# Kernel tuning notes

Hardware: AMD Instinct MI355X
Metric: run time of the kernel (lower is better)

The kernel has to match this reference:

```python
import jax, jax.numpy as jnp
import numpy as np
from jax import lax

S, L = 8192, 16
N_WORD, N_CHAR = 50000, 128
WORD_DIM, CHAR_DIM = 256, 64
WORD_HID, CHAR_HID = 512, 128
N_TAG = 64


def _lstm_gates(x, h, Wih, Whh, bih, bhh):
    # x: [..., D], h: [..., H]; torch gate order: i, f, g, o
    g = x @ Wih.T + h @ Whh.T + bih + bhh
    i, f, gg, o = jnp.split(g, 4, axis=-1)
    return jax.nn.sigmoid(i), jax.nn.sigmoid(f), jnp.tanh(gg), jax.nn.sigmoid(o)


def setup_inputs() -> dict:
    key = jax.random.key(0)
    ks = jax.random.split(key, 16)
    sc = 0.1
    inp = {
        'x': jax.random.randint(ks[0], (S,), 0, N_WORD),
        'chars': jax.random.randint(ks[1], (S, L), 0, N_CHAR),
        'lengths': jax.random.randint(ks[2], (S,), 0, L),
        'word_emb': jax.random.normal(ks[3], (N_WORD, WORD_DIM), jnp.float32) * sc,
        'char_emb': jax.random.normal(ks[4], (N_CHAR, CHAR_DIM), jnp.float32) * sc,
        'c_Wih': jax.random.normal(ks[5], (4 * CHAR_HID, CHAR_DIM), jnp.float32) * sc,
        'c_Whh': jax.random.normal(ks[6], (4 * CHAR_HID, CHAR_HID), jnp.float32) * sc,
        'c_bih': jax.random.normal(ks[7], (4 * CHAR_HID,), jnp.float32) * sc,
        'c_bhh': jax.random.normal(ks[8], (4 * CHAR_HID,), jnp.float32) * sc,
        'w_Wih': jax.random.normal(ks[9], (4 * WORD_HID, WORD_DIM + CHAR_HID), jnp.float32) * sc,
        'w_Whh': jax.random.normal(ks[10], (4 * WORD_HID, WORD_HID), jnp.float32) * sc,
        'w_bih': jax.random.normal(ks[11], (4 * WORD_HID,), jnp.float32) * sc,
        'w_bhh': jax.random.normal(ks[12], (4 * WORD_HID,), jnp.float32) * sc,
        'lin_W': jax.random.normal(ks[13], (N_TAG, WORD_HID), jnp.float32) * sc,
        'lin_b': jax.random.normal(ks[14], (N_TAG,), jnp.float32) * sc,
    }
    return inp


def _char_features(chars, lengths, char_emb, Wih, Whh, bih, bhh):
    # batched char LSTM over all S words at once; returns final CELL state (h[1] in torch)
    emb = char_emb[chars]              # [S, L, char_dim]
    xs = jnp.swapaxes(emb, 0, 1)       # [L, S, char_dim]
    h0 = jnp.zeros((chars.shape[0], CHAR_HID), emb.dtype)
    c0 = jnp.zeros_like(h0)

    def step(carry, inp):
        h, c = carry
        x_t, t = inp
        i, f, g, o = _lstm_gates(x_t, h, Wih, Whh, bih, bhh)
        c_new = f * c + i * g
        h_new = o * jnp.tanh(c_new)
        m = (t < lengths)[:, None]     # only update within each word's true length
        return (jnp.where(m, h_new, h), jnp.where(m, c_new, c)), None

    (h, c), _ = lax.scan(step, (h0, c0), (xs, jnp.arange(L)))
    return c                            # [S, char_hidden]


def _word_lstm(seq, Wih, Whh, bih, bhh):
    # seq: [S, D] single sequence (batch=1 in original)
    h0 = jnp.zeros((WORD_HID,), seq.dtype)
    c0 = jnp.zeros_like(h0)

    def step(carry, x_t):
        h, c = carry
        i, f, g, o = _lstm_gates(x_t, h, Wih, Whh, bih, bhh)
        c = f * c + i * g
        h = o * jnp.tanh(c)
        return (h, c), h

    _, hs = lax.scan(step, (h0, c0), seq)
    return hs                           # [S, word_hidden]


def reference(x, chars, lengths, word_emb, char_emb,
              c_Wih, c_Whh, c_bih, c_bhh,
              w_Wih, w_Whh, w_bih, w_bhh,
              lin_W, lin_b):
    char_feat = _char_features(chars, lengths, char_emb, c_Wih, c_Whh, c_bih, c_bhh)
    we = word_emb[x]                                    # [S, word_dim]
    seq = jnp.concatenate([we, char_feat], axis=1)      # [S, word_dim+char_hidden]
    hs = _word_lstm(seq, w_Wih, w_Whh, w_bih, w_bhh)    # [S, word_hidden]
    logits = hs @ lin_W.T + lin_b                       # [S, n_tag]
    return jax.nn.log_softmax(logits, axis=1)
```

## Files before the change

### kernel.cpp

```cpp
#include <hip/hip_runtime.h>
#include <hip/hip_bf16.h>

#define S_LEN 8192
#define CLEN 16
#define WDIM 256
#define CDIM 64
#define CHID 128
#define WHID 512
#define GDIM 2048
#define NTAG 64
#define KDIM 384
#define NWG 32

typedef unsigned long long u64;

__device__ __forceinline__ float sigmoidf_(float x) {
  return 1.0f / (1.0f + __expf(-x));
}
__device__ __forceinline__ float tanhf_(float x) {
  return 1.0f - 2.0f / (__expf(2.0f * x) + 1.0f);
}

__global__ __launch_bounds__(256)
void char_lstm_kernel(const int* __restrict__ chars, const int* __restrict__ lengths,
                      const float* __restrict__ emb, const float* __restrict__ Wih,
                      const float* __restrict__ Whh, const float* __restrict__ bih,
                      const float* __restrict__ bhh, float* __restrict__ cf)
{
  __shared__ float xs[16][CDIM];
  __shared__ float hsm[16][CHID];
  __shared__ int cidx[16];
  __shared__ int lens[16];
  const int tid = threadIdx.x;
  const int grp = tid >> 7;
  const int j = tid & 127;
  const int wb = blockIdx.x * 16;

  for (int i = tid; i < 16 * CHID; i += 256) (&hsm[0][0])[i] = 0.f;
  if (tid < 16) lens[tid] = lengths[wb + tid];
  float c[8];
#pragma unroll
  for (int w = 0; w < 8; ++w) c[w] = 0.f;
  const float bi = bih[j] + bhh[j];
  const float bf = bih[CHID + j] + bhh[CHID + j];
  const float bg = bih[2 * CHID + j] + bhh[2 * CHID + j];
  const float bo = bih[3 * CHID + j] + bhh[3 * CHID + j];

  for (int t = 0; t < CLEN; ++t) {
    __syncthreads();
    if (tid < 16) cidx[tid] = chars[(wb + tid) * CLEN + t];
    __syncthreads();
    {
      int e = tid * 4;
      int wi = e >> 6;
      int k = e & 63;
      const float4 v = *(const float4*)(emb + (size_t)cidx[wi] * CDIM + k);
      *(float4*)(&xs[wi][k]) = v;
    }
    __syncthreads();
    float ai[8], af[8], ag[8], ao[8];
#pragma unroll
    for (int w = 0; w < 8; ++w) { ai[w] = bi; af[w] = bf; ag[w] = bg; ao[w] = bo; }
    for (int k = 0; k < CDIM; k += 4) {
      float4 w0 = *(const float4*)(Wih + (size_t)j * CDIM + k);
      float4 w1 = *(const float4*)(Wih + (size_t)(CHID + j) * CDIM + k);
      float4 w2 = *(const float4*)(Wih + (size_t)(2 * CHID + j) * CDIM + k);
      float4 w3 = *(const float4*)(Wih + (size_t)(3 * CHID + j) * CDIM + k);
#pragma unroll
      for (int s = 0; s < 4; ++s) {
        float wiv = (&w0.x)[s], wfv = (&w1.x)[s], wgv = (&w2.x)[s], wov = (&w3.x)[s];
#pragma unroll
        for (int w = 0; w < 8; ++w) {
          float xv = xs[grp * 8 + w][k + s];
          ai[w] = fmaf(wiv, xv, ai[w]);
          af[w] = fmaf(wfv, xv, af[w]);
          ag[w] = fmaf(wgv, xv, ag[w]);
          ao[w] = fmaf(wov, xv, ao[w]);
        }
      }
    }
    for (int k = 0; k < CHID; k += 4) {
      float4 w0 = *(const float4*)(Whh + (size_t)j * CHID + k);
      float4 w1 = *(const float4*)(Whh + (size_t)(CHID + j) * CHID + k);
      float4 w2 = *(const float4*)(Whh + (size_t)(2 * CHID + j) * CHID + k);
      float4 w3 = *(const float4*)(Whh + (size_t)(3 * CHID + j) * CHID + k);
#pragma unroll
      for (int s = 0; s < 4; ++s) {
        float wiv = (&w0.x)[s], wfv = (&w1.x)[s], wgv = (&w2.x)[s], wov = (&w3.x)[s];
#pragma unroll
        for (int w = 0; w < 8; ++w) {
          float hv = hsm[grp * 8 + w][k + s];
          ai[w] = fmaf(wiv, hv, ai[w]);
          af[w] = fmaf(wfv, hv, af[w]);
          ag[w] = fmaf(wgv, hv, ag[w]);
          ao[w] = fmaf(wov, hv, ao[w]);
        }
      }
    }
    __syncthreads();
#pragma unroll
    for (int w = 0; w < 8; ++w) {
      if (t < lens[grp * 8 + w]) {
        float iv = sigmoidf_(ai[w]);
        float fv = sigmoidf_(af[w]);
        float gv = tanhf_(ag[w]);
        float ov = sigmoidf_(ao[w]);
        c[w] = fv * c[w] + iv * gv;
        hsm[grp * 8 + w][j] = ov * tanhf_(c[w]);
      }
    }
  }
#pragma unroll
  for (int w = 0; w < 8; ++w)
    cf[(size_t)(wb + grp * 8 + w) * CHID + j] = c[w];
}

#define BM 64
#define BN 64
#define BK 32
__global__ __launch_bounds__(256)
void gx_gemm_kernel(const int* __restrict__ x, const float* __restrict__ word_emb,
                    const float* __restrict__ char_feat, const float* __restrict__ Wih,
                    const float* __restrict__ bih, const float* __restrict__ bhh,
                    float* __restrict__ Gx)
{
  __shared__ float As[BK][BM + 1];
  __shared__ float Bs[BK][BN + 1];
  __shared__ int xidx[BM];
  const int tid = threadIdx.x;
  const int tx = tid & 15, ty = tid >> 4;
  const int m0 = blockIdx.y * BM;
  const int n0 = blockIdx.x * BN;
  if (tid < BM) xidx[tid] = x[m0 + tid];
  float acc[4][4] = {};
  for (int k0 = 0; k0 < KDIM; k0 += BK) {
    __syncthreads();
    {
      int i = tid >> 5;
      int kk = tid & 31;
#pragma unroll
      for (int l = 0; l < 8; ++l) {
        int row = i + l * 8;
        int k = k0 + kk;
        int tt = m0 + row;
        float v = (k < WDIM) ? word_emb[(size_t)xidx[row] * WDIM + k]
                             : char_feat[(size_t)tt * CHID + (k - WDIM)];
        As[kk][row] = v;
      }
    }
    {
      int jjj = tid >> 5;
      int kk = tid & 31;
#pragma unroll
      for (int l = 0; l < 8; ++l) {
        int col = jjj + l * 8;
        Bs[kk][col] = Wih[(size_t)(n0 + col) * KDIM + k0 + kk];
      }
    }
    __syncthreads();
#pragma unroll
    for (int kk = 0; kk < BK; ++kk) {
      float a[4], b[4];
#pragma unroll
      for (int m = 0; m < 4; ++m) a[m] = As[kk][ty * 4 + m];
#pragma unroll
      for (int n = 0; n < 4; ++n) b[n] = Bs[kk][tx * 4 + n];
#pragma unroll
      for (int m = 0; m < 4; ++m)
#pragma unroll
        for (int n = 0; n < 4; ++n)
          acc[m][n] = fmaf(a[m], b[n], acc[m][n]);
    }
  }
#pragma unroll
  for (int n = 0; n < 4; ++n) {
    int g = n0 + tx * 4 + n;
    float bias = bih[g] + bhh[g];
#pragma unroll
    for (int m = 0; m < 4; ++m) {
      int tt = m0 + ty * 4 + m;
      Gx[(size_t)tt * GDIM + g] = acc[m][n] + bias;
    }
  }
}

__global__ __launch_bounds__(256, 1)
void word_lstm_seq(const float* __restrict__ Whh, const float* __restrict__ Gx,
                   float* __restrict__ hs, u64* hbuf)
{
  __shared__ float h_lds[WHID];
  __shared__ float red[2][256];
  const int tid = threadIdx.x;
  const int wg = blockIdx.x;
  const int cc = tid >> 6;
  const int lane = tid & 63;
  const int kb = cc * 128;

  const int grow = (lane >> 4) * WHID + wg * 16 + (lane & 15);
  float wl[128];
  {
    const float* wsrc = Whh + (size_t)grow * WHID + kb;
#pragma unroll
    for (int k = 0; k < 128; ++k) wl[k] = wsrc[k];
  }

  float c_state = 0.f;

  for (int t = 0; t < S_LEN; ++t) {
    float gxv = 0.f;
    if (tid < 64)
      gxv = Gx[(size_t)t * GDIM + grow];
    if (t > 0) {
      const u64* base = hbuf + (size_t)(t & 1) * WHID + kb;
      const int s0 = 2 * lane;
      u64 a, b;
      const unsigned want = (unsigned)t;
      while (true) {
        a = __hip_atomic_load(base + s0, __ATOMIC_RELAXED,
                              __HIP_MEMORY_SCOPE_AGENT);
        b = __hip_atomic_load(base + s0 + 1, __ATOMIC_RELAXED,
                              __HIP_MEMORY_SCOPE_AGENT);
        if ((unsigned)(a >> 32) == want && (unsigned)(b >> 32) == want) break;
      }
      float2 hv2 = make_float2(__uint_as_float((unsigned)a),
                               __uint_as_float((unsigned)b));
      *(float2*)(&h_lds[kb + s0]) = hv2;
    } else {
      *(float2*)(&h_lds[kb + 2 * lane]) = make_float2(0.f, 0.f);
    }
    __threadfence_block();
    float acc = 0.f;
#pragma unroll
    for (int g = 0; g < 32; ++g) {
      float4 hv = *(const float4*)(&h_lds[kb + 4 * g]);
      acc = fmaf(wl[4 * g + 0], hv.x, acc);
      acc = fmaf(wl[4 * g + 1], hv.y, acc);
      acc = fmaf(wl[4 * g + 2], hv.z, acc);
      acc = fmaf(wl[4 * g + 3], hv.w, acc);
    }
    red[t & 1][tid] = acc;
    __syncthreads();
    if (tid < 64) {
      const float* rp = &red[t & 1][0];
      float s = rp[tid] + rp[64 + tid] + rp[128 + tid] + rp[192 + tid] + gxv;
      float act = ((tid >> 4) == 2) ? tanhf_(s) : sigmoidf_(s);
      int jj = tid & 15;
      float iv = __shfl(act, jj);
      float fv = __shfl(act, 16 + jj);
      float gv = __shfl(act, 32 + jj);
      float ov = __shfl(act, 48 + jj);
      if (tid < 16) {
        c_state = fv * c_state + iv * gv;
        float hv = ov * tanhf_(c_state);
        const int hidx = wg * 16 + tid;
        u64 pkt = ((u64)(unsigned)(t + 1) << 32) | (u64)__float_as_uint(hv);
        (void)__hip_atomic_exchange(
            &hbuf[(size_t)((t + 1) & 1) * WHID + hidx], pkt,
            __ATOMIC_RELAXED, __HIP_MEMORY_SCOPE_AGENT);
        hs[(size_t)t * WHID + hidx] = hv;
      }
    }
  }
}

__global__ __launch_bounds__(256)
void tag_kernel(const float* __restrict__ hs, const float* __restrict__ W,
                const float* __restrict__ b, float* __restrict__ out)
{
  const int wave = threadIdx.x >> 6;
  const int lane = threadIdx.x & 63;
  const int t = blockIdx.x * 4 + wave;
  const float* hr = hs + (size_t)t * WHID;
  const float* wr = W + (size_t)lane * WHID;
  float acc = b[lane];
  for (int k = 0; k < WHID; k += 4) {
    float4 wv = *(const float4*)(wr + k);
    float4 hv = *(const float4*)(hr + k);
    acc = fmaf(wv.x, hv.x, acc);
    acc = fmaf(wv.y, hv.y, acc);
    acc = fmaf(wv.z, hv.z, acc);
    acc = fmaf(wv.w, hv.w, acc);
  }
  float m = acc;
#pragma unroll
  for (int off = 32; off > 0; off >>= 1) m = fmaxf(m, __shfl_xor(m, off));
  float e = __expf(acc - m);
  float sum = e;
#pragma unroll
  for (int off = 32; off > 0; off >>= 1) sum += __shfl_xor(sum, off);
  out[(size_t)t * NTAG + lane] = (acc - m) - __logf(sum);
}

extern "C" void kernel_launch(void* const* d_in, const int* in_sizes, int n_in,
                              void* d_out, int out_size, void* d_ws, size_t ws_size,
                              hipStream_t stream)
{
  const int* x          = (const int*)d_in[0];
  const int* chars      = (const int*)d_in[1];
  const int* lengths    = (const int*)d_in[2];
  const float* word_emb = (const float*)d_in[3];
  const float* char_emb = (const float*)d_in[4];
  const float* c_Wih    = (const float*)d_in[5];
  const float* c_Whh    = (const float*)d_in[6];
  const float* c_bih    = (const float*)d_in[7];
  const float* c_bhh    = (const float*)d_in[8];
  const float* w_Wih    = (const float*)d_in[9];
  const float* w_Whh    = (const float*)d_in[10];
  const float* w_bih    = (const float*)d_in[11];
  const float* w_bhh    = (const float*)d_in[12];
  const float* lin_W    = (const float*)d_in[13];
  const float* lin_b    = (const float*)d_in[14];
  float* out = (float*)d_out;

  char* ws = (char*)d_ws;
  u64*   hbuf      = (u64*)ws;
  float* char_feat = (float*)(ws + 8192);
  float* Gx        = (float*)(ws + 8192 + (size_t)S_LEN * CHID * 4);
  float* hs        = (float*)(ws + 8192 + (size_t)S_LEN * CHID * 4
                                        + (size_t)S_LEN * GDIM * 4);

  hipMemsetAsync(ws, 0, 8192, stream);

  char_lstm_kernel<<<S_LEN / 16, 256, 0, stream>>>(
      chars, lengths, char_emb, c_Wih, c_Whh, c_bih, c_bhh, char_feat);

  dim3 g2(GDIM / BN, S_LEN / BM);
  gx_gemm_kernel<<<g2, 256, 0, stream>>>(
      x, word_emb, char_feat, w_Wih, w_bih, w_bhh, Gx);

  word_lstm_seq<<<NWG, 256, 0, stream>>>(w_Whh, Gx, hs, hbuf);

  tag_kernel<<<S_LEN / 4, 256, 0, stream>>>(hs, lin_W, lin_b, out);
}
```

Baseline: 15.86 ms.

## Restructure word LSTM recurrence so each wave owns full gate rows with shuffle reduction

Measured after the change: 19.80 ms. 24.9% more time.

```diff
diff --git a/kernel.cpp b/kernel.cpp
--- a/kernel.cpp
+++ b/kernel.cpp
@@ -188,77 +188,80 @@
 void word_lstm_seq(const float* __restrict__ Whh, const float* __restrict__ Gx,
                    float* __restrict__ hs, u64* hbuf)
 {
-  __shared__ float h_lds[WHID];
-  __shared__ float red[2][256];
-  const int tid = threadIdx.x;
-  const int wg = blockIdx.x;
-  const int cc = tid >> 6;
+  __shared__ __align__(16) float stg[2][640];
+  const int tid  = threadIdx.x;
+  const int wg   = blockIdx.x;
+  const int wv   = tid >> 6;
   const int lane = tid & 63;
-  const int kb = cc * 128;
-
-  const int grow = (lane >> 4) * WHID + wg * 16 + (lane & 15);
-  float wl[128];
+  const int kc   = lane >> 4;
+  const int r    = lane & 15;
+  const int q    = r >> 2;
+  const int u    = r & 3;
+  const int grow = q * WHID + wg * 16 + wv * 4 + u;
+
+  float4 w_[32];
   {
-    const float* wsrc = Whh + (size_t)grow * WHID + kb;
-#pragma unroll
-    for (int k = 0; k < 128; ++k) wl[k] = wsrc[k];
+    const float* wsrc = Whh + (size_t)grow * WHID + 128 * kc;
+#pragma unroll
+    for (int i = 0; i < 32; ++i) {
+      const int fo = (4 * kc + 4 * i) & 127;
+      w_[i] = *(const float4*)(wsrc + fo);
+    }
+#pragma unroll
+    for (int i = 0; i < 32; ++i)
+      asm volatile("" : "+v"(w_[i].x), "+v"(w_[i].y), "+v"(w_[i].z), "+v"(w_[i].w));
   }
 
   float c_state = 0.f;
 
   for (int t = 0; t < S_LEN; ++t) {
-    float gxv = 0.f;
-    if (tid < 64)
-      gxv = Gx[(size_t)t * GDIM + grow];
+    const int par = t & 1;
+    float gxv = Gx[(size_t)t * GDIM + grow];
+    float v0, v1;
     if (t > 0) {
-      const u64* base = hbuf + (size_t)(t & 1) * WHID + kb;
-      const int s0 = 2 * lane;
+      const u64* pb = hbuf + (size_t)par * WHID + 128 * wv + 2 * lane;
+      const unsigned want = (unsigned)t;
       u64 a, b;
-      const unsigned want = (unsigned)t;
-      while (true) {
-        a = __hip_atomic_load(base + s0, __ATOMIC_RELAXED,
-                              __HIP_MEMORY_SCOPE_AGENT);
-        b = __hip_atomic_load(base + s0 + 1, __ATOMIC_RELAXED,
-                              __HIP_MEMORY_SCOPE_AGENT);
-        if ((unsigned)(a >> 32) == want && (unsigned)(b >> 32) == want) break;
-      }
-      float2 hv2 = make_float2(__uint_as_float((unsigned)a),
-                               __uint_as_float((unsigned)b));
-      *(float2*)(&h_lds[kb + s0]) = hv2;
-    } else {
-      *(float2*)(&h_lds[kb + 2 * lane]) = make_float2(0.f, 0.f);
-    }
-    __threadfence_block();
+      do {
+        a = __hip_atomic_load(pb + 0, __ATOMIC_RELAXED, __HIP_MEMORY_SCOPE_AGENT);
+        b = __hip_atomic_load(pb + 1, __ATOMIC_RELAXED, __HIP_MEMORY_SCOPE_AGENT);
+      } while (((unsigned)(a >> 32) != want) | ((unsigned)(b >> 32) != want));
+      v0 = __uint_as_float((unsigned)a);
+      v1 = __uint_as_float((unsigned)b);
+    } else { v0 = 0.f; v1 = 0.f; }
+    {
+      float* cb = &stg[par][148 * wv];
+      *(float2*)(cb + 2 * lane) = make_float2(v0, v1);
+      if (lane < 6) *(float2*)(cb + 128 + 2 * lane) = make_float2(v0, v1);
+    }
+    __syncthreads();
+    const float* rdp = &stg[par][152 * kc];
     float acc = 0.f;
 #pragma unroll
-    for (int g = 0; g < 32; ++g) {
-      float4 hv = *(const float4*)(&h_lds[kb + 4 * g]);
-      acc = fmaf(wl[4 * g + 0], hv.x, acc);
-      acc = fmaf(wl[4 * g + 1], hv.y, acc);
-      acc = fmaf(wl[4 * g + 2], hv.z, acc);
-      acc = fmaf(wl[4 * g + 3], hv.w, acc);
-    }
-    red[t & 1][tid] = acc;
-    __syncthreads();
-    if (tid < 64) {
-      const float* rp = &red[t & 1][0];
-      float s = rp[tid] + rp[64 + tid] + rp[128 + tid] + rp[192 + tid] + gxv;
-      float act = ((tid >> 4) == 2) ? tanhf_(s) : sigmoidf_(s);
-      int jj = tid & 15;
-      float iv = __shfl(act, jj);
-      float fv = __shfl(act, 16 + jj);
-      float gv = __shfl(act, 32 + jj);
-      float ov = __shfl(act, 48 + jj);
-      if (tid < 16) {
-        c_state = fv * c_state + iv * gv;
-        float hv = ov * tanhf_(c_state);
-        const int hidx = wg * 16 + tid;
-        u64 pkt = ((u64)(unsigned)(t + 1) << 32) | (u64)__float_as_uint(hv);
-        (void)__hip_atomic_exchange(
-            &hbuf[(size_t)((t + 1) & 1) * WHID + hidx], pkt,
-            __ATOMIC_RELAXED, __HIP_MEMORY_SCOPE_AGENT);
-        hs[(size_t)t * WHID + hidx] = hv;
-      }
+    for (int i = 0; i < 32; ++i) {
+      const float4 hv = *(const float4*)(rdp + 4 * i);
+      acc = fmaf(w_[i].x, hv.x, acc);
+      acc = fmaf(w_[i].y, hv.y, acc);
+      acc = fmaf(w_[i].z, hv.z, acc);
+      acc = fmaf(w_[i].w, hv.w, acc);
+    }
+    acc += __shfl_xor(acc, 16);
+    acc += __shfl_xor(acc, 32);
+    const float s = acc + gxv;
+    const float act = (q == 2) ? tanhf_(s) : sigmoidf_(s);
+    const int gb = lane & 48;
+    const float iv = __shfl(act, gb + u);
+    const float fv = __shfl(act, gb + 4 + u);
+    const float gv = __shfl(act, gb + 8 + u);
+    const float ov = __shfl(act, gb + 12 + u);
+    c_state = fv * c_state + iv * gv;
+    const float hv = ov * tanhf_(c_state);
+    if (lane < 4) {
+      const int hidx = wg * 16 + wv * 4 + lane;
+      const u64 pkt = ((u64)(unsigned)(t + 1) << 32) | (u64)__float_as_uint(hv);
+      (void)__hip_atomic_exchange(&hbuf[(size_t)((t + 1) & 1) * WHID + hidx], pkt,
+                                  __ATOMIC_RELAXED, __HIP_MEMORY_SCOPE_AGENT);
+      hs[(size_t)t * WHID + hidx] = hv;
     }
   }
 }
```

## Race redundant XCC-local LSTM replicas against global group for faster h exchange

Applied to the files above, without the earlier changes.

Measured after the change: 17.90 ms. 1.13x slower.

```diff
diff --git a/kernel.cpp b/kernel.cpp
--- a/kernel.cpp
+++ b/kernel.cpp
@@ -186,80 +186,186 @@
 
 __global__ __launch_bounds__(256, 1)
 void word_lstm_seq(const float* __restrict__ Whh, const float* __restrict__ Gx,
-                   float* __restrict__ hs, u64* hbuf)
+                   float* __restrict__ hs, u64* hbufG, u64* hbufL,
+                   int* tickets, int* done_cnt, int* done)
 {
+  __shared__ __align__(16) float4 wlds[4096];
   __shared__ float h_lds[WHID];
   __shared__ float red[2][256];
+  __shared__ int wg_s, loc_s, bail_s;
   const int tid = threadIdx.x;
-  const int wg = blockIdx.x;
-  const int cc = tid >> 6;
+  const int bid = blockIdx.x;
+
+  if (tid == 0) {
+    bail_s = 0;
+    int myid, loc;
+    if (bid < NWG) {
+      myid = bid; loc = -1;
+    } else {
+      unsigned xcc;
+      asm volatile("s_getreg_b32 %0, hwreg(HW_REG_XCC_ID)" : "=s"(xcc));
+      xcc &= 15u;
+      int tk = __hip_atomic_fetch_add(&tickets[xcc], 1, __ATOMIC_RELAXED,
+                                      __HIP_MEMORY_SCOPE_AGENT);
+      myid = -1; loc = (int)xcc;
+      if (tk < NWG) {
+        for (int i = 0; i < 30000; ++i) {
+          if (__hip_atomic_load(&tickets[xcc], __ATOMIC_RELAXED,
+                                __HIP_MEMORY_SCOPE_AGENT) >= NWG) {
+            myid = tk; break;
+          }
+        }
+      }
+    }
+    wg_s = myid; loc_s = loc;
+  }
+  __syncthreads();
+  const int wg = wg_s;
+  if (wg < 0) return;
+  const bool local = (loc_s >= 0);
+  u64* __restrict__ mybuf = local ? (hbufL + (size_t)loc_s * 1024) : hbufG;
+
+  const int cc   = tid >> 6;
   const int lane = tid & 63;
-  const int kb = cc * 128;
-
+  const int kb   = cc * 128;
   const int grow = (lane >> 4) * WHID + wg * 16 + (lane & 15);
-  float wl[128];
+
+  for (int L = tid; L < 4096; L += 256) {
+    int g = L >> 8;
+    int rem = L & 255;
+    int c2 = rem >> 6;
+    int r = rem & 63;
+    int gr = (r >> 4) * WHID + wg * 16 + (r & 15);
+    wlds[L] = *(const float4*)(Whh + (size_t)gr * WHID + c2 * 128 + 4 * g);
+  }
+  float4 wr_[16];
   {
-    const float* wsrc = Whh + (size_t)grow * WHID + kb;
-#pragma unroll
-    for (int k = 0; k < 128; ++k) wl[k] = wsrc[k];
-  }
+    const float* wsrc2 = Whh + (size_t)grow * WHID + kb + 64;
+#pragma unroll
+    for (int i = 0; i < 16; ++i) wr_[i] = *(const float4*)(wsrc2 + 4 * i);
+  }
+  __syncthreads();
 
   float c_state = 0.f;
+  int lmode = local ? 1 : 0;
 
   for (int t = 0; t < S_LEN; ++t) {
+    const int par = t & 1;
     float gxv = 0.f;
     if (tid < 64)
       gxv = Gx[(size_t)t * GDIM + grow];
+    float v0 = 0.f, v1 = 0.f;
     if (t > 0) {
-      const u64* base = hbuf + (size_t)(t & 1) * WHID + kb;
-      const int s0 = 2 * lane;
-      u64 a, b;
       const unsigned want = (unsigned)t;
-      while (true) {
-        a = __hip_atomic_load(base + s0, __ATOMIC_RELAXED,
-                              __HIP_MEMORY_SCOPE_AGENT);
-        b = __hip_atomic_load(base + s0 + 1, __ATOMIC_RELAXED,
-                              __HIP_MEMORY_SCOPE_AGENT);
-        if ((unsigned)(a >> 32) == want && (unsigned)(b >> 32) == want) break;
-      }
-      float2 hv2 = make_float2(__uint_as_float((unsigned)a),
-                               __uint_as_float((unsigned)b));
-      *(float2*)(&h_lds[kb + s0]) = hv2;
-    } else {
-      *(float2*)(&h_lds[kb + 2 * lane]) = make_float2(0.f, 0.f);
-    }
+      const size_t soff = (size_t)par * WHID + kb + 2 * lane;
+      bool found = false;
+      if (lmode) {
+        const u64* pL = mybuf + soff;
+        int iter = 0;
+        for (;;) {
+          int4 rr;
+          asm volatile("global_load_dwordx4 %0, %1, off sc0\n\t"
+                       "s_waitcnt vmcnt(0)"
+                       : "=v"(rr) : "v"(pL) : "memory");
+          if ((unsigned)rr.y == want && (unsigned)rr.w == want) {
+            v0 = __int_as_float(rr.x); v1 = __int_as_float(rr.z);
+            found = true; break;
+          }
+          ++iter;
+          if (t == 1 && iter >= 4096) { lmode = 0; break; }
+          if ((iter & 15) == 0 &&
+              __hip_atomic_load(done, __ATOMIC_RELAXED,
+                                __HIP_MEMORY_SCOPE_AGENT)) {
+            bail_s = 1; found = true; break;
+          }
+        }
+      }
+      if (!found) {
+        const u64* pG = hbufG + soff;
+        const u64* pL = mybuf + soff;
+        int iter = 0;
+        for (;;) {
+          u64 a = __hip_atomic_load(pG + 0, __ATOMIC_RELAXED,
+                                    __HIP_MEMORY_SCOPE_AGENT);
+          u64 b = __hip_atomic_load(pG + 1, __ATOMIC_RELAXED,
+                                    __HIP_MEMORY_SCOPE_AGENT);
+          if ((unsigned)(a >> 32) == want && (unsigned)(b >> 32) == want) {
+            v0 = __uint_as_float((unsigned)a);
+            v1 = __uint_as_float((unsigned)b);
+            break;
+          }
+          if (local) {
+            int4 rr;
+            asm volatile("global_load_dwordx4 %0, %1, off sc0\n\t"
+                         "s_waitcnt vmcnt(0)"
+                         : "=v"(rr) : "v"(pL) : "memory");
+            if ((unsigned)rr.y == want && (unsigned)rr.w == want) {
+              v0 = __int_as_float(rr.x); v1 = __int_as_float(rr.z); break;
+            }
+          }
+          if (((++iter) & 15) == 0 &&
+              __hip_atomic_load(done, __ATOMIC_RELAXED,
+                                __HIP_MEMORY_SCOPE_AGENT)) {
+            bail_s = 1; break;
+          }
+        }
+      }
+    }
+    *(float2*)(&h_lds[kb + 2 * lane]) = make_float2(v0, v1);
     __threadfence_block();
     float acc = 0.f;
 #pragma unroll
-    for (int g = 0; g < 32; ++g) {
-      float4 hv = *(const float4*)(&h_lds[kb + 4 * g]);
-      acc = fmaf(wl[4 * g + 0], hv.x, acc);
-      acc = fmaf(wl[4 * g + 1], hv.y, acc);
-      acc = fmaf(wl[4 * g + 2], hv.z, acc);
-      acc = fmaf(wl[4 * g + 3], hv.w, acc);
-    }
-    red[t & 1][tid] = acc;
-    __syncthreads();
+    for (int g = 0; g < 16; ++g) {
+      const float4 wv = wlds[g * 256 + cc * 64 + lane];
+      const float4 hv = *(const float4*)(&h_lds[kb + 4 * g]);
+      acc = fmaf(wv.x, hv.x, acc);
+      acc = fmaf(wv.y, hv.y, acc);
+      acc = fmaf(wv.z, hv.z, acc);
+      acc = fmaf(wv.w, hv.w, acc);
+    }
+#pragma unroll
+    for (int i = 0; i < 16; ++i) {
+      const float4 hv = *(const float4*)(&h_lds[kb + 64 + 4 * i]);
+      acc = fmaf(wr_[i].x, hv.x, acc);
+      acc = fmaf(wr_[i].y, hv.y, acc);
+      acc = fmaf(wr_[i].z, hv.z, acc);
+      acc = fmaf(wr_[i].w, hv.w, acc);
+    }
+    red[par][tid] = acc;
+    __syncthreads();
+    if (bail_s) break;
     if (tid < 64) {
-      const float* rp = &red[t & 1][0];
-      float s = rp[tid] + rp[64 + tid] + rp[128 + tid] + rp[192 + tid] + gxv;
-      float act = ((tid >> 4) == 2) ? tanhf_(s) : sigmoidf_(s);
-      int jj = tid & 15;
+      const float* rp = red[par];
+      float s = rp[lane] + rp[64 + lane] + rp[128 + lane] + rp[192 + lane] + gxv;
+      float act = ((lane >> 4) == 2) ? tanhf_(s) : sigmoidf_(s);
+      int jj = lane & 15;
       float iv = __shfl(act, jj);
       float fv = __shfl(act, 16 + jj);
       float gv = __shfl(act, 32 + jj);
       float ov = __shfl(act, 48 + jj);
-      if (tid < 16) {
+      if (lane < 16) {
         c_state = fv * c_state + iv * gv;
         float hv = ov * tanhf_(c_state);
-        const int hidx = wg * 16 + tid;
-        u64 pkt = ((u64)(unsigned)(t + 1) << 32) | (u64)__float_as_uint(hv);
-        (void)__hip_atomic_exchange(
-            &hbuf[(size_t)((t + 1) & 1) * WHID + hidx], pkt,
-            __ATOMIC_RELAXED, __HIP_MEMORY_SCOPE_AGENT);
+        const int hidx = wg * 16 + lane;
+        const u64 pkt = ((u64)(unsigned)(t + 1) << 32) | (u64)__float_as_uint(hv);
+        const size_t off = (size_t)((t + 1) & 1) * WHID + hidx;
+        if (local)
+          (void)__hip_atomic_exchange(mybuf + off, pkt, __ATOMIC_RELAXED,
+                                      __HIP_MEMORY_SCOPE_WORKGROUP);
+        else
+          (void)__hip_atomic_exchange(mybuf + off, pkt, __ATOMIC_RELAXED,
+                                      __HIP_MEMORY_SCOPE_AGENT);
         hs[(size_t)t * WHID + hidx] = hv;
       }
     }
+  }
+
+  if (tid == 0 && !bail_s) {
+    const int gidx = local ? loc_s : 16;
+    int r = __hip_atomic_fetch_add(&done_cnt[gidx], 1, __ATOMIC_RELAXED,
+                                   __HIP_MEMORY_SCOPE_AGENT);
+    if (r == NWG - 1)
+      __hip_atomic_store(done, 1, __ATOMIC_RELEASE, __HIP_MEMORY_SCOPE_AGENT);
   }
 }
 
@@ -313,13 +419,17 @@
   float* out = (float*)d_out;
 
   char* ws = (char*)d_ws;
-  u64*   hbuf      = (u64*)ws;
-  float* char_feat = (float*)(ws + 8192);
-  float* Gx        = (float*)(ws + 8192 + (size_t)S_LEN * CHID * 4);
-  float* hs        = (float*)(ws + 8192 + (size_t)S_LEN * CHID * 4
-                                        + (size_t)S_LEN * GDIM * 4);
-
-  hipMemsetAsync(ws, 0, 8192, stream);
+  int*   tickets   = (int*)ws;
+  int*   done_cnt  = (int*)(ws + 64);
+  int*   done      = (int*)(ws + 132);
+  u64*   hbufG     = (u64*)(ws + 4096);
+  u64*   hbufL     = (u64*)(ws + 16384);
+  float* char_feat = (float*)(ws + 147456);
+  float* Gx        = (float*)(ws + 147456 + (size_t)S_LEN * CHID * 4);
+  float* hs        = (float*)(ws + 147456 + (size_t)S_LEN * CHID * 4
+                                          + (size_t)S_LEN * GDIM * 4);
+
+  hipMemsetAsync(ws, 0, 147456, stream);
 
   char_lstm_kernel<<<S_LEN / 16, 256, 0, stream>>>(
       chars, lengths, char_emb, c_Wih, c_Whh, c_bih, c_bhh, char_feat);
@@ -328,7 +438,8 @@
   gx_gemm_kernel<<<g2, 256, 0, stream>>>(
       x, word_emb, char_feat, w_Wih, w_bih, w_bhh, Gx);
 
-  word_lstm_seq<<<NWG, 256, 0, stream>>>(w_Whh, Gx, hs, hbuf);
+  word_lstm_seq<<<320, 256, 0, stream>>>(w_Whh, Gx, hs, hbufG, hbufL,
+                                         tickets, done_cnt, done);
 
   tag_kernel<<<S_LEN / 4, 256, 0, stream>>>(hs, lin_W, lin_b, out);
 }
```

## Pipeline h polling with double inline-asm probes and split Whh between LDS and cache

Applied to the files above, without the earlier changes.

Result: slower. 18.23 ms (+15.0%).

```diff
diff --git a/kernel.cpp b/kernel.cpp
--- a/kernel.cpp
+++ b/kernel.cpp
@@ -188,60 +188,106 @@
 void word_lstm_seq(const float* __restrict__ Whh, const float* __restrict__ Gx,
                    float* __restrict__ hs, u64* hbuf)
 {
+  __shared__ __align__(16) float4 wlds4[16 * 256];
   __shared__ float h_lds[WHID];
   __shared__ float red[2][256];
-  const int tid = threadIdx.x;
-  const int wg = blockIdx.x;
-  const int cc = tid >> 6;
+  const int tid  = threadIdx.x;
+  const int wg   = blockIdx.x;
+  const int cc   = tid >> 6;
   const int lane = tid & 63;
-  const int kb = cc * 128;
-
+  const int kb   = cc * 128;
   const int grow = (lane >> 4) * WHID + wg * 16 + (lane & 15);
-  float wl[128];
+
   {
     const float* wsrc = Whh + (size_t)grow * WHID + kb;
 #pragma unroll
-    for (int k = 0; k < 128; ++k) wl[k] = wsrc[k];
-  }
+    for (int j = 0; j < 16; ++j)
+      wlds4[j * 256 + tid] = *(const float4*)(wsrc + 4 * j);
+  }
+  const float* __restrict__ wsrc2 = Whh + (size_t)grow * WHID + kb + 64;
+  __syncthreads();
 
   float c_state = 0.f;
+  int use_probes = 1;
 
   for (int t = 0; t < S_LEN; ++t) {
-    float gxv = 0.f;
-    if (tid < 64)
-      gxv = Gx[(size_t)t * GDIM + grow];
+    const int par = t & 1;
+    float4 wr_[16];
+#pragma unroll
+    for (int i = 0; i < 16; ++i) wr_[i] = *(const float4*)(wsrc2 + 4 * i);
+    float gxv = Gx[(size_t)t * GDIM + grow];
+    float v0 = 0.f, v1 = 0.f;
+    int4 pa = {0, 0, 0, 0}, pb = {0, 0, 0, 0};
     if (t > 0) {
-      const u64* base = hbuf + (size_t)(t & 1) * WHID + kb;
-      const int s0 = 2 * lane;
-      u64 a, b;
       const unsigned want = (unsigned)t;
-      while (true) {
-        a = __hip_atomic_load(base + s0, __ATOMIC_RELAXED,
-                              __HIP_MEMORY_SCOPE_AGENT);
-        b = __hip_atomic_load(base + s0 + 1, __ATOMIC_RELAXED,
-                              __HIP_MEMORY_SCOPE_AGENT);
-        if ((unsigned)(a >> 32) == want && (unsigned)(b >> 32) == want) break;
-      }
-      float2 hv2 = make_float2(__uint_as_float((unsigned)a),
-                               __uint_as_float((unsigned)b));
-      *(float2*)(&h_lds[kb + s0]) = hv2;
-    } else {
-      *(float2*)(&h_lds[kb + 2 * lane]) = make_float2(0.f, 0.f);
-    }
+      const u64* ps = hbuf + (size_t)par * WHID + kb + 2 * lane;
+      bool ok = false;
+      int4 rr = {0, 0, 0, 0};
+      if (use_probes) {
+        asm volatile("global_load_dwordx4 %0, %1, off sc0 sc1"
+                     : "=&v"(pa) : "v"(ps) : "memory");
+        asm volatile("global_load_dwordx4 %0, %1, off sc0 sc1"
+                     : "=&v"(pb) : "v"(ps) : "memory");
+        int miss = 0;
+        for (;;) {
+          asm volatile("s_waitcnt vmcnt(1)" ::: "memory");
+          __builtin_amdgcn_sched_barrier(0);
+          if ((unsigned)pa.y == want && (unsigned)pa.w == want) {
+            rr = pa; ok = true; break;
+          }
+          asm volatile("global_load_dwordx4 %0, %1, off sc0 sc1"
+                       : "=&v"(pa) : "v"(ps) : "memory");
+          asm volatile("s_waitcnt vmcnt(1)" ::: "memory");
+          __builtin_amdgcn_sched_barrier(0);
+          if ((unsigned)pb.y == want && (unsigned)pb.w == want) {
+            rr = pb; ok = true; break;
+          }
+          asm volatile("global_load_dwordx4 %0, %1, off sc0 sc1"
+                       : "=&v"(pb) : "v"(ps) : "memory");
+          if (++miss >= 256) { use_probes = 0; break; }
+        }
+      }
+      if (!ok) {
+        u64 a, b;
+        do {
+          a = __hip_atomic_load(ps + 0, __ATOMIC_RELAXED, __HIP_MEMORY_SCOPE_AGENT);
+          b = __hip_atomic_load(ps + 1, __ATOMIC_RELAXED, __HIP_MEMORY_SCOPE_AGENT);
+        } while (((unsigned)(a >> 32) != want) | ((unsigned)(b >> 32) != want));
+        v0 = __uint_as_float((unsigned)a);
+        v1 = __uint_as_float((unsigned)b);
+      } else {
+        v0 = __int_as_float(rr.x);
+        v1 = __int_as_float(rr.z);
+      }
+    }
+    *(float2*)(&h_lds[kb + 2 * lane]) = make_float2(v0, v1);
     __threadfence_block();
     float acc = 0.f;
 #pragma unroll
-    for (int g = 0; g < 32; ++g) {
-      float4 hv = *(const float4*)(&h_lds[kb + 4 * g]);
-      acc = fmaf(wl[4 * g + 0], hv.x, acc);
-      acc = fmaf(wl[4 * g + 1], hv.y, acc);
-      acc = fmaf(wl[4 * g + 2], hv.z, acc);
-      acc = fmaf(wl[4 * g + 3], hv.w, acc);
-    }
-    red[t & 1][tid] = acc;
-    __syncthreads();
+    for (int j = 0; j < 16; ++j) {
+      const float4 wv = wlds4[j * 256 + tid];
+      const float4 hv = *(const float4*)(&h_lds[kb + 4 * j]);
+      acc = fmaf(wv.x, hv.x, acc);
+      acc = fmaf(wv.y, hv.y, acc);
+      acc = fmaf(wv.z, hv.z, acc);
+      acc = fmaf(wv.w, hv.w, acc);
+    }
+#pragma unroll
+    for (int i = 0; i < 16; ++i) {
+      const float4 hv = *(const float4*)(&h_lds[kb + 64 + 4 * i]);
+      acc = fmaf(wr_[i].x, hv.x, acc);
+      acc = fmaf(wr_[i].y, hv.y, acc);
+      acc = fmaf(wr_[i].z, hv.z, acc);
+      acc = fmaf(wr_[i].w, hv.w, acc);
+    }
+    red[par][tid] = acc;
+    asm volatile("" :: "v"(pa.x), "v"(pa.y), "v"(pa.z), "v"(pa.w),
+                       "v"(pb.x), "v"(pb.y), "v"(pb.z), "v"(pb.w));
+    asm volatile("s_waitcnt vmcnt(0)" ::: "memory");
+    asm volatile("s_waitcnt lgkmcnt(0)" ::: "memory");
+    __builtin_amdgcn_s_barrier();
     if (tid < 64) {
-      const float* rp = &red[t & 1][0];
+      const float* rp = red[par];
       float s = rp[tid] + rp[64 + tid] + rp[128 + tid] + rp[192 + tid] + gxv;
       float act = ((tid >> 4) == 2) ? tanhf_(s) : sigmoidf_(s);
       int jj = tid & 15;
@@ -253,10 +299,10 @@
         c_state = fv * c_state + iv * gv;
         float hv = ov * tanhf_(c_state);
         const int hidx = wg * 16 + tid;
-        u64 pkt = ((u64)(unsigned)(t + 1) << 32) | (u64)__float_as_uint(hv);
-        (void)__hip_atomic_exchange(
-            &hbuf[(size_t)((t + 1) & 1) * WHID + hidx], pkt,
-            __ATOMIC_RELAXED, __HIP_MEMORY_SCOPE_AGENT);
+        const u64 pkt = ((u64)(unsigned)(t + 1) << 32) | (u64)__float_as_uint(hv);
+        (void)__hip_atomic_exchange(&hbuf[(size_t)((t + 1) & 1) * WHID + hidx],
+                                    pkt, __ATOMIC_RELAXED,
+                                    __HIP_MEMORY_SCOPE_AGENT);
         hs[(size_t)t * WHID + hidx] = hv;
       }
     }
```
